# Kernel tuning notes

Measured on AMD Instinct MI355X. Metric: run time of the kernel, lower is better.

The kernel has to match this reference:

```python
import jax, jax.numpy as jnp
import numpy as np

RADIUS = 1.0
NSAMPLE = 1024  # num_votes
EPS = 1e-5     # BatchNorm eps


def _bn2(x, gamma, beta):
    # BatchNorm over [B, C, NS]: stats per channel across (batch, sample)
    m = jnp.mean(x, axis=(0, 2), keepdims=True)
    v = jnp.var(x, axis=(0, 2), keepdims=True)
    return gamma[None, :, None] * (x - m) * jax.lax.rsqrt(v + EPS) + beta[None, :, None]


def _bn1(x, gamma, beta):
    # BatchNorm over [B, C] (conv1d head with length 1): stats across batch
    m = jnp.mean(x, axis=0, keepdims=True)
    v = jnp.var(x, axis=0, keepdims=True)
    return gamma[None, :] * (x - m) * jax.lax.rsqrt(v + EPS) + beta[None, :]


def setup_inputs() -> dict:
    key = jax.random.key(0)
    ks = jax.random.split(key, 16)
    B, N, C = 8, 65536, 256
    def w(k, o, i):
        return jax.random.normal(k, (o, i), jnp.float32) * (1.0 / np.sqrt(i))
    inp = {
        'xyz': jax.random.normal(ks[0], (B, N, 3), jnp.float32),
        'features': jax.random.normal(ks[1], (B, C, N), jnp.float32),
        # shared MLP (conv2d 1x1 + BN + ReLU) x3, input channels = C+3 (use_xyz)
        'w1': w(ks[2], 128, C + 3), 'b1': jnp.zeros(128), 'g1': jnp.ones(128), 'be1': jnp.zeros(128),
        'w2': w(ks[3], 128, 128),   'b2': jnp.zeros(128), 'g2': jnp.ones(128), 'be2': jnp.zeros(128),
        'w3': w(ks[4], 128, 128),   'b3': jnp.zeros(128), 'g3': jnp.ones(128), 'be3': jnp.zeros(128),
        # conv1d head
        'hw1': w(ks[5], 128, 128), 'hb1': jnp.zeros(128), 'hg1': jnp.ones(128), 'hbe1': jnp.zeros(128),
        'hw2': w(ks[6], 128, 128), 'hb2': jnp.zeros(128), 'hg2': jnp.ones(128), 'hbe2': jnp.zeros(128),
        'hw3': w(ks[7], 12, 128),  'hb3': jnp.zeros(12),
    }
    return inp


def reference(xyz, features, w1, b1, g1, be1, w2, b2, g2, be2, w3, b3, g3, be3,
              hw1, hb1, hg1, hbe1, hw2, hb2, hg2, hbe2, hw3, hb3):
    B, N, _ = xyz.shape
    # FPS with npoint=1 deterministically selects point 0
    center = xyz[:, 0, :]                                   # [B,3]
    d2 = jnp.sum((xyz - center[:, None, :]) ** 2, axis=-1)   # [B,N]
    mask = d2 < RADIUS * RADIUS
    ar = jnp.arange(N)
    # ball query: first NSAMPLE in-radius indices (index order), pad with first hit
    order = jnp.argsort(jnp.where(mask, ar, N + ar), axis=1)[:, :NSAMPLE]  # [B,NS]
    valid = jnp.take_along_axis(mask, order, axis=1)
    inds = jnp.where(valid, order, order[:, :1])              # [B,NS]
    g_xyz = (jnp.take_along_axis(xyz, inds[:, :, None], axis=1) - center[:, None, :]) / RADIUS  # [B,NS,3]
    g_feat = jax.vmap(lambda f, i: f[:, i])(features, inds)    # [B,C,NS]
    g = jnp.concatenate([jnp.swapaxes(g_xyz, 1, 2), g_feat], axis=1)  # [B,C+3,NS]

    def mlp(x, w, b, gm, bt):
        y = jnp.einsum('oc,bcn->bon', w, x) + b[None, :, None]
        return jax.nn.relu(_bn2(y, gm, bt))

    h = mlp(g, w1, b1, g1, be1)
    h = mlp(h, w2, b2, g2, be2)
    h = mlp(h, w3, b3, g3, be3)
    f = jnp.max(h, axis=2)                                    # [B,128] maxpool over nsample

    net = jax.nn.relu(_bn1(f @ hw1.T + hb1, hg1, hbe1))
    net = jax.nn.relu(_bn1(net @ hw2.T + hb2, hg2, hbe2))
    net = net @ hw3.T + hb3                                   # [B,12]

    center_out = center + net[:, 0:3]
    size = net[:, 3:6]
    rot_6d = net[:, 6:12]
    return (center_out, size, rot_6d)
```

## Files before the change

### kernel.cpp

```cpp
#include <hip/hip_runtime.h>
#include <hip/hip_bf16.h>
#include <stdint.h>

#define BATCH 8
#define NPTS  65536
#define CFEAT 256
#define K1    259
#define CH    128
#define NS    1024
#define EPSF  1e-5f
#define INVN  (1.0f / (BATCH * NS))

__device__ __forceinline__ unsigned fenc(float f) {
  unsigned u = __float_as_uint(f);
  return (u & 0x80000000u) ? ~u : (u | 0x80000000u);
}
__device__ __forceinline__ float fdec(unsigned k) {
  unsigned u = (k & 0x80000000u) ? (k & 0x7fffffffu) : ~k;
  return __uint_as_float(u);
}

__global__ __launch_bounds__(1024) void k_select(const float* __restrict__ xyz,
                                                 int* __restrict__ inds,
                                                 float* __restrict__ center) {
  int b = blockIdx.x;
  int tid = threadIdx.x;
  int lane = tid & 63, wid = tid >> 6;
  const float* xb = xyz + (size_t)b * NPTS * 3;
  float cx = xb[0], cy = xb[1], cz = xb[2];
  if (tid < 3) center[b * 3 + tid] = xb[tid];

  __shared__ int wcnt[16];
  int total = 0;
  int* ib = inds + b * NS;

  for (int base = 0; base < NPTS; base += 1024) {
    int i = base + tid;
    float dx = xb[(size_t)i * 3 + 0] - cx;
    float dy = xb[(size_t)i * 3 + 1] - cy;
    float dz = xb[(size_t)i * 3 + 2] - cz;
    float d2 = dx * dx + dy * dy + dz * dz;
    bool pred = d2 < 1.0f;
    unsigned long long bal = __ballot(pred);
    if (lane == 0) wcnt[wid] = (int)__popcll(bal);
    __syncthreads();
    int woff = 0, itot = 0;
#pragma unroll
    for (int w = 0; w < 16; ++w) {
      int c = wcnt[w];
      if (w < wid) woff += c;
      itot += c;
    }
    int pos = total + woff + (int)__popcll(bal & ((1ull << lane) - 1ull));
    if (pred && pos < NS) ib[pos] = i;
    total += itot;
    __syncthreads();
    if (total >= NS) break;
  }
  for (int j = total + tid; j < NS; j += 1024) ib[j] = 0;
}

__global__ __launch_bounds__(256) void k_gather(const float* __restrict__ xyz,
                                                const float* __restrict__ feat,
                                                const int* __restrict__ inds,
                                                const float* __restrict__ center,
                                                float* __restrict__ G) {
  int rk = blockIdx.x;
  int b = rk / K1, k = rk - b * K1;
  const int* ib = inds + b * NS;
  float* gr = G + (size_t)rk * NS;
  if (k < 3) {
    float cv = center[b * 3 + k];
    const float* xb = xyz + (size_t)b * NPTS * 3;
    for (int j = threadIdx.x; j < NS; j += 256)
      gr[j] = xb[(size_t)ib[j] * 3 + k] - cv;
  } else {
    const float* fr = feat + ((size_t)b * CFEAT + (k - 3)) * NPTS;
    for (int j = threadIdx.x; j < NS; j += 256)
      gr[j] = fr[ib[j]];
  }
}

__device__ __forceinline__ void store_and_stats(float* __restrict__ yb,
                                                float* __restrict__ sums,
                                                const float* __restrict__ bias,
                                                float acc[4][4],
                                                int n0, int tx, int ty) {
#pragma unroll
  for (int r = 0; r < 4; ++r) {
    int o = ty * 4 + r;
    float bs = bias[o];
    float4 v = make_float4(acc[r][0] + bs, acc[r][1] + bs,
                           acc[r][2] + bs, acc[r][3] + bs);
    *(float4*)&yb[(size_t)o * NS + n0 + tx * 4] = v;
    float s = v.x + v.y + v.z + v.w;
    float q = v.x * v.x + v.y * v.y + v.z * v.z + v.w * v.w;
    s += __shfl_xor(s, 1, 64); q += __shfl_xor(q, 1, 64);
    s += __shfl_xor(s, 2, 64); q += __shfl_xor(q, 2, 64);
    s += __shfl_xor(s, 4, 64); q += __shfl_xor(q, 4, 64);
    if (tx == 0) {
      atomicAdd(&sums[o], s);
      atomicAdd(&sums[CH + o], q);
    }
  }
}

__global__ __launch_bounds__(256) void k_gemm1(const float* __restrict__ G,
                                               const float* __restrict__ W,
                                               const float* __restrict__ bias,
                                               float* __restrict__ y,
                                               float* __restrict__ sums) {
  __shared__ float Ws[32][132];
  __shared__ float Xs[32][36];
  int b = blockIdx.y;
  int n0 = blockIdx.x * 32;
  int tid = threadIdx.x;

  int tx = tid & 7, ty = tid >> 3;
  float acc[4][4];
#pragma unroll
  for (int r = 0; r < 4; ++r)
#pragma unroll
    for (int j = 0; j < 4; ++j) acc[r][j] = 0.f;

  const float* Gb = G + (size_t)b * K1 * NS;

  for (int k0 = 0; k0 < K1; k0 += 32) {
#pragma unroll
    for (int i = 0; i < 16; ++i) {
      int e = tid + 256 * i;
      int o = e >> 5, kk = e & 31;
      int k = k0 + kk;
      Ws[kk][o] = (k < K1) ? W[o * K1 + k] : 0.f;
    }
#pragma unroll
    for (int i = 0; i < 4; ++i) {
      int e = tid + 256 * i;
      int kk = e >> 5, j = e & 31;
      int k = k0 + kk;
      Xs[kk][j] = (k < K1) ? Gb[(size_t)k * NS + n0 + j] : 0.f;
    }
    __syncthreads();
#pragma unroll
    for (int kk = 0; kk < 32; ++kk) {
      float4 xv = *(const float4*)&Xs[kk][tx * 4];
      float4 wv = *(const float4*)&Ws[kk][ty * 4];
      acc[0][0] += wv.x * xv.x; acc[0][1] += wv.x * xv.y; acc[0][2] += wv.x * xv.z; acc[0][3] += wv.x * xv.w;
      acc[1][0] += wv.y * xv.x; acc[1][1] += wv.y * xv.y; acc[1][2] += wv.y * xv.z; acc[1][3] += wv.y * xv.w;
      acc[2][0] += wv.z * xv.x; acc[2][1] += wv.z * xv.y; acc[2][2] += wv.z * xv.z; acc[2][3] += wv.z * xv.w;
      acc[3][0] += wv.w * xv.x; acc[3][1] += wv.w * xv.y; acc[3][2] += wv.w * xv.z; acc[3][3] += wv.w * xv.w;
    }
    __syncthreads();
  }
  store_and_stats(y + (size_t)b * CH * NS, sums, bias, acc, n0, tx, ty);
}

template <bool LAST>
__global__ __launch_bounds__(256) void k_gemm23(const float* __restrict__ x,
                                                const float* __restrict__ sums_prev,
                                                const float* __restrict__ gamma,
                                                const float* __restrict__ beta,
                                                const float* __restrict__ W,
                                                const float* __restrict__ bias,
                                                float* __restrict__ y,
                                                float* __restrict__ sums_out,
                                                unsigned* __restrict__ maxk,
                                                unsigned* __restrict__ mink) {
  __shared__ float Ws[32][132];
  __shared__ float Xs[32][36];
  __shared__ float scl[CH], shf[CH];
  int b = blockIdx.y;
  int n0 = blockIdx.x * 32;
  int tid = threadIdx.x;
  if (tid < CH) {
    float s = sums_prev[tid], q = sums_prev[CH + tid];
    float mean = s * INVN;
    float var = fmaxf(q * INVN - mean * mean, 0.f);
    float sc = gamma[tid] * rsqrtf(var + EPSF);
    scl[tid] = sc;
    shf[tid] = beta[tid] - mean * sc;
  }
  __syncthreads();

  int tx = tid & 7, ty = tid >> 3;
  float acc[4][4];
#pragma unroll
  for (int r = 0; r < 4; ++r)
#pragma unroll
    for (int j = 0; j < 4; ++j) acc[r][j] = 0.f;

  const float* xb = x + (size_t)b * CH * NS;

  for (int k0 = 0; k0 < CH; k0 += 32) {
#pragma unroll
    for (int i = 0; i < 16; ++i) {
      int e = tid + 256 * i;
      int o = e >> 5, kk = e & 31;
      Ws[kk][o] = W[o * CH + k0 + kk];
    }
#pragma unroll
    for (int i = 0; i < 4; ++i) {
      int e = tid + 256 * i;
      int kk = e >> 5, j = e & 31;
      int k = k0 + kk;
      float v = xb[(size_t)k * NS + n0 + j];
      Xs[kk][j] = fmaxf(scl[k] * v + shf[k], 0.f);
    }
    __syncthreads();
#pragma unroll
    for (int kk = 0; kk < 32; ++kk) {
      float4 xv = *(const float4*)&Xs[kk][tx * 4];
      float4 wv = *(const float4*)&Ws[kk][ty * 4];
      acc[0][0] += wv.x * xv.x; acc[0][1] += wv.x * xv.y; acc[0][2] += wv.x * xv.z; acc[0][3] += wv.x * xv.w;
      acc[1][0] += wv.y * xv.x; acc[1][1] += wv.y * xv.y; acc[1][2] += wv.y * xv.z; acc[1][3] += wv.y * xv.w;
      acc[2][0] += wv.z * xv.x; acc[2][1] += wv.z * xv.y; acc[2][2] += wv.z * xv.z; acc[2][3] += wv.z * xv.w;
      acc[3][0] += wv.w * xv.x; acc[3][1] += wv.w * xv.y; acc[3][2] += wv.w * xv.z; acc[3][3] += wv.w * xv.w;
    }
    __syncthreads();
  }

  if (!LAST) {
    store_and_stats(y + (size_t)b * CH * NS, sums_out, bias, acc, n0, tx, ty);
  } else {
#pragma unroll
    for (int r = 0; r < 4; ++r) {
      int o = ty * 4 + r;
      float bs = bias[o];
      float4 v = make_float4(acc[r][0] + bs, acc[r][1] + bs,
                             acc[r][2] + bs, acc[r][3] + bs);
      float s = v.x + v.y + v.z + v.w;
      float q = v.x * v.x + v.y * v.y + v.z * v.z + v.w * v.w;
      float mx = fmaxf(fmaxf(v.x, v.y), fmaxf(v.z, v.w));
      float mn = fminf(fminf(v.x, v.y), fminf(v.z, v.w));
      s += __shfl_xor(s, 1, 64); q += __shfl_xor(q, 1, 64);
      mx = fmaxf(mx, __shfl_xor(mx, 1, 64)); mn = fminf(mn, __shfl_xor(mn, 1, 64));
      s += __shfl_xor(s, 2, 64); q += __shfl_xor(q, 2, 64);
      mx = fmaxf(mx, __shfl_xor(mx, 2, 64)); mn = fminf(mn, __shfl_xor(mn, 2, 64));
      s += __shfl_xor(s, 4, 64); q += __shfl_xor(q, 4, 64);
      mx = fmaxf(mx, __shfl_xor(mx, 4, 64)); mn = fminf(mn, __shfl_xor(mn, 4, 64));
      if (tx == 0) {
        atomicAdd(&sums_out[o], s);
        atomicAdd(&sums_out[CH + o], q);
        atomicMax(&maxk[b * CH + o], fenc(mx));
        atomicMin(&mink[b * CH + o], fenc(mn));
      }
    }
  }
}

__global__ __launch_bounds__(128) void k_head(const float* __restrict__ sums3,
                                              const float* __restrict__ ga3, const float* __restrict__ be3,
                                              const unsigned* __restrict__ maxk, const unsigned* __restrict__ mink,
                                              const float* __restrict__ hw1, const float* __restrict__ hb1,
                                              const float* __restrict__ hg1, const float* __restrict__ hbe1,
                                              const float* __restrict__ hw2, const float* __restrict__ hb2,
                                              const float* __restrict__ hg2, const float* __restrict__ hbe2,
                                              const float* __restrict__ hw3, const float* __restrict__ hb3,
                                              const float* __restrict__ center,
                                              float* __restrict__ out) {
  __shared__ float A[BATCH * 128];
  __shared__ float Bm[BATCH * 128];
  int c = threadIdx.x;
  {
    float s = sums3[c], q = sums3[CH + c];
    float mean = s * INVN;
    float var = fmaxf(q * INVN - mean * mean, 0.f);
    float sc = ga3[c] * rsqrtf(var + EPSF);
    float sh = be3[c] - mean * sc;
#pragma unroll
    for (int b = 0; b < BATCH; ++b) {
      float ymax = fdec(maxk[b * CH + c]);
      float ymin = fdec(mink[b * CH + c]);
      float ye = (sc >= 0.f) ? ymax : ymin;
      A[b * 128 + c] = fmaxf(sc * ye + sh, 0.f);
    }
  }
  __syncthreads();

  {
    float v[BATCH];
    float bs = hb1[c];
#pragma unroll
    for (int b = 0; b < BATCH; ++b) v[b] = bs;
    const float4* w4 = (const float4*)hw1 + c * 32;
    for (int k4 = 0; k4 < 32; ++k4) {
      float4 w = w4[k4];
#pragma unroll
      for (int b = 0; b < BATCH; ++b) {
        const float* Ar = &A[b * 128 + k4 * 4];
        v[b] += Ar[0] * w.x + Ar[1] * w.y + Ar[2] * w.z + Ar[3] * w.w;
      }
    }
    float m = 0.f;
#pragma unroll
    for (int b = 0; b < BATCH; ++b) m += v[b];
    m *= (1.f / BATCH);
    float var = 0.f;
#pragma unroll
    for (int b = 0; b < BATCH; ++b) { float d = v[b] - m; var += d * d; }
    var *= (1.f / BATCH);
    float r = rsqrtf(var + EPSF);
    float ga = hg1[c], be = hbe1[c];
#pragma unroll
    for (int b = 0; b < BATCH; ++b)
      Bm[b * 128 + c] = fmaxf(ga * (v[b] - m) * r + be, 0.f);
  }
  __syncthreads();

  {
    float v[BATCH];
    float bs = hb2[c];
#pragma unroll
    for (int b = 0; b < BATCH; ++b) v[b] = bs;
    const float4* w4 = (const float4*)hw2 + c * 32;
    for (int k4 = 0; k4 < 32; ++k4) {
      float4 w = w4[k4];
#pragma unroll
      for (int b = 0; b < BATCH; ++b) {
        const float* Br = &Bm[b * 128 + k4 * 4];
        v[b] += Br[0] * w.x + Br[1] * w.y + Br[2] * w.z + Br[3] * w.w;
      }
    }
    float m = 0.f;
#pragma unroll
    for (int b = 0; b < BATCH; ++b) m += v[b];
    m *= (1.f / BATCH);
    float var = 0.f;
#pragma unroll
    for (int b = 0; b < BATCH; ++b) { float d = v[b] - m; var += d * d; }
    var *= (1.f / BATCH);
    float r = rsqrtf(var + EPSF);
    float ga = hg2[c], be = hbe2[c];
#pragma unroll
    for (int b = 0; b < BATCH; ++b)
      A[b * 128 + c] = fmaxf(ga * (v[b] - m) * r + be, 0.f);
  }
  __syncthreads();

  if (c < 96) {
    int b = c / 12, j = c % 12;
    float o = hb3[j];
    const float4* w4 = (const float4*)hw3 + j * 32;
    for (int k4 = 0; k4 < 32; ++k4) {
      float4 w = w4[k4];
      const float* Ar = &A[b * 128 + k4 * 4];
      o += Ar[0] * w.x + Ar[1] * w.y + Ar[2] * w.z + Ar[3] * w.w;
    }
    if (j < 3)      out[b * 3 + j] = center[b * 3 + j] + o;
    else if (j < 6) out[24 + b * 3 + (j - 3)] = o;
    else            out[48 + b * 6 + (j - 6)] = o;
  }
}

extern "C" void kernel_launch(void* const* d_in, const int* in_sizes, int n_in,
                              void* d_out, int out_size, void* d_ws, size_t ws_size,
                              hipStream_t stream) {
  const float* xyz  = (const float*)d_in[0];
  const float* feat = (const float*)d_in[1];
  const float* w1   = (const float*)d_in[2];
  const float* b1   = (const float*)d_in[3];
  const float* ga1  = (const float*)d_in[4];
  const float* be1  = (const float*)d_in[5];
  const float* w2   = (const float*)d_in[6];
  const float* b2   = (const float*)d_in[7];
  const float* ga2  = (const float*)d_in[8];
  const float* be2  = (const float*)d_in[9];
  const float* w3   = (const float*)d_in[10];
  const float* b3   = (const float*)d_in[11];
  const float* ga3  = (const float*)d_in[12];
  const float* be3  = (const float*)d_in[13];
  const float* hw1  = (const float*)d_in[14];
  const float* hb1  = (const float*)d_in[15];
  const float* hg1  = (const float*)d_in[16];
  const float* hbe1 = (const float*)d_in[17];
  const float* hw2  = (const float*)d_in[18];
  const float* hb2  = (const float*)d_in[19];
  const float* hg2  = (const float*)d_in[20];
  const float* hbe2 = (const float*)d_in[21];
  const float* hw3  = (const float*)d_in[22];
  const float* hb3  = (const float*)d_in[23];
  float* out = (float*)d_out;

  char* ws = (char*)d_ws;
  size_t off = 0;
  auto alloc = [&](size_t bytes) -> void* {
    void* p = ws + off;
    off = (off + bytes + 255) & ~(size_t)255;
    return p;
  };
  float*    sums1 = (float*)alloc(2 * CH * 4);
  float*    sums2 = (float*)alloc(2 * CH * 4);
  float*    sums3 = (float*)alloc(2 * CH * 4);
  unsigned* maxk  = (unsigned*)alloc((size_t)BATCH * CH * 4);
  unsigned* mink  = (unsigned*)alloc((size_t)BATCH * CH * 4);
  int*      inds  = (int*)alloc((size_t)BATCH * NS * 4);
  float*    center= (float*)alloc(BATCH * 3 * 4);
  float*    G     = (float*)alloc((size_t)BATCH * K1 * NS * 4);
  float*    y1    = (float*)alloc((size_t)BATCH * CH * NS * 4);
  float*    y2    = (float*)alloc((size_t)BATCH * CH * NS * 4);

  hipMemsetAsync(sums1, 0, (size_t)((char*)mink - (char*)sums1), stream);
  hipMemsetAsync(mink, 0xFF, (size_t)BATCH * CH * 4, stream);

  k_select<<<dim3(BATCH), dim3(1024), 0, stream>>>(xyz, inds, center);
  k_gather<<<dim3(BATCH * K1), dim3(256), 0, stream>>>(xyz, feat, inds, center, G);
  k_gemm1<<<dim3(NS / 32, BATCH), dim3(256), 0, stream>>>(G, w1, b1, y1, sums1);
  k_gemm23<false><<<dim3(NS / 32, BATCH), dim3(256), 0, stream>>>(y1, sums1, ga1, be1,
                                                                  w2, b2, y2, sums2,
                                                                  nullptr, nullptr);
  k_gemm23<true><<<dim3(NS / 32, BATCH), dim3(256), 0, stream>>>(y2, sums2, ga2, be2,
                                                                 w3, b3, nullptr, sums3,
                                                                 maxk, mink);
  k_head<<<dim3(1), dim3(128), 0, stream>>>(sums3, ga3, be3, maxk, mink,
                                            hw1, hb1, hg1, hbe1,
                                            hw2, hb2, hg2, hbe2, hw3, hb3,
                                            center, out);
}
```

Baseline: 872.1 us.

## Fuse point gather into first GEMM and fold workspace init into select

Removes the separate gather kernel and the intermediate G buffer. k_gemm1 now gathers the xyz offsets and feature columns for its 32 samples directly into a full-K shared tile, padded to 288 rows. The two memsets are replaced by zero/fill stores done in block 0 of k_select. k_gemm23 also preloads its whole normalized input tile into shared memory once, instead of reloading it per K slice. This saves the G write and read and two launches. In exchange, the random feature gathers run inside only 256 GEMM blocks, which have less latency hiding, and the larger shared-memory footprint may lower occupancy.

New measurement: 851.4 us. 1.02x faster.

```diff
diff --git a/kernel.cpp b/kernel.cpp
--- a/kernel.cpp
+++ b/kernel.cpp
@@ -6,6 +6,7 @@
 #define NPTS  65536
 #define CFEAT 256
 #define K1    259
+#define K1PAD 288
 #define CH    128
 #define NS    1024
 #define EPSF  1e-5f
@@ -22,10 +23,19 @@
 
 __global__ __launch_bounds__(1024) void k_select(const float* __restrict__ xyz,
                                                  int* __restrict__ inds,
-                                                 float* __restrict__ center) {
+                                                 float* __restrict__ center,
+                                                 float* __restrict__ sums,
+                                                 unsigned* __restrict__ maxk,
+                                                 unsigned* __restrict__ mink) {
   int b = blockIdx.x;
   int tid = threadIdx.x;
   int lane = tid & 63, wid = tid >> 6;
+
+  if (b == 0) {
+    if (tid < 3 * 2 * CH) sums[tid] = 0.f;
+    if (tid < BATCH * CH) { maxk[tid] = 0u; mink[tid] = 0xFFFFFFFFu; }
+  }
+
   const float* xb = xyz + (size_t)b * NPTS * 3;
   float cx = xb[0], cy = xb[1], cz = xb[2];
   if (tid < 3) center[b * 3 + tid] = xb[tid];
@@ -58,27 +68,6 @@
     if (total >= NS) break;
   }
   for (int j = total + tid; j < NS; j += 1024) ib[j] = 0;
-}
-
-__global__ __launch_bounds__(256) void k_gather(const float* __restrict__ xyz,
-                                                const float* __restrict__ feat,
-                                                const int* __restrict__ inds,
-                                                const float* __restrict__ center,
-                                                float* __restrict__ G) {
-  int rk = blockIdx.x;
-  int b = rk / K1, k = rk - b * K1;
-  const int* ib = inds + b * NS;
-  float* gr = G + (size_t)rk * NS;
-  if (k < 3) {
-    float cv = center[b * 3 + k];
-    const float* xb = xyz + (size_t)b * NPTS * 3;
-    for (int j = threadIdx.x; j < NS; j += 256)
-      gr[j] = xb[(size_t)ib[j] * 3 + k] - cv;
-  } else {
-    const float* fr = feat + ((size_t)b * CFEAT + (k - 3)) * NPTS;
-    for (int j = threadIdx.x; j < NS; j += 256)
-      gr[j] = fr[ib[j]];
-  }
 }
 
 __device__ __forceinline__ void store_and_stats(float* __restrict__ yb,
@@ -105,16 +94,41 @@
   }
 }
 
-__global__ __launch_bounds__(256) void k_gemm1(const float* __restrict__ G,
+__global__ __launch_bounds__(256) void k_gemm1(const float* __restrict__ xyz,
+                                               const float* __restrict__ feat,
+                                               const int* __restrict__ inds,
+                                               const float* __restrict__ center,
                                                const float* __restrict__ W,
                                                const float* __restrict__ bias,
                                                float* __restrict__ y,
                                                float* __restrict__ sums) {
   __shared__ float Ws[32][132];
-  __shared__ float Xs[32][36];
+  __shared__ float Xs[K1PAD][36];
+  __shared__ int   ids[32];
+  __shared__ float cenl[3];
   int b = blockIdx.y;
   int n0 = blockIdx.x * 32;
   int tid = threadIdx.x;
+  if (tid < 32) ids[tid] = inds[b * NS + n0 + tid];
+  if (tid < 3)  cenl[tid] = center[b * 3 + tid];
+  __syncthreads();
+
+  const float* featb = feat + (size_t)b * CFEAT * NPTS;
+  const float* xyzb  = xyz + (size_t)b * NPTS * 3;
+
+  if (tid < 96) {
+    int k = tid >> 5, j = tid & 31;
+    Xs[k][j] = xyzb[(size_t)ids[j] * 3 + k] - cenl[k];
+  }
+#pragma unroll 8
+  for (int e = tid; e < CFEAT * 32; e += 256) {
+    int k = e >> 5, j = e & 31;
+    Xs[3 + k][j] = featb[(size_t)k * NPTS + ids[j]];
+  }
+#pragma unroll
+  for (int e = tid; e < 29 * 32; e += 256) {
+    Xs[K1 + (e >> 5)][e & 31] = 0.f;
+  }
 
   int tx = tid & 7, ty = tid >> 3;
   float acc[4][4];
@@ -123,9 +137,7 @@
 #pragma unroll
     for (int j = 0; j < 4; ++j) acc[r][j] = 0.f;
 
-  const float* Gb = G + (size_t)b * K1 * NS;
-
-  for (int k0 = 0; k0 < K1; k0 += 32) {
+  for (int k0 = 0; k0 < K1PAD; k0 += 32) {
 #pragma unroll
     for (int i = 0; i < 16; ++i) {
       int e = tid + 256 * i;
@@ -133,17 +145,10 @@
       int k = k0 + kk;
       Ws[kk][o] = (k < K1) ? W[o * K1 + k] : 0.f;
     }
-#pragma unroll
-    for (int i = 0; i < 4; ++i) {
-      int e = tid + 256 * i;
-      int kk = e >> 5, j = e & 31;
-      int k = k0 + kk;
-      Xs[kk][j] = (k < K1) ? Gb[(size_t)k * NS + n0 + j] : 0.f;
-    }
     __syncthreads();
 #pragma unroll
     for (int kk = 0; kk < 32; ++kk) {
-      float4 xv = *(const float4*)&Xs[kk][tx * 4];
+      float4 xv = *(const float4*)&Xs[k0 + kk][tx * 4];
       float4 wv = *(const float4*)&Ws[kk][ty * 4];
       acc[0][0] += wv.x * xv.x; acc[0][1] += wv.x * xv.y; acc[0][2] += wv.x * xv.z; acc[0][3] += wv.x * xv.w;
       acc[1][0] += wv.y * xv.x; acc[1][1] += wv.y * xv.y; acc[1][2] += wv.y * xv.z; acc[1][3] += wv.y * xv.w;
@@ -167,7 +172,7 @@
                                                 unsigned* __restrict__ maxk,
                                                 unsigned* __restrict__ mink) {
   __shared__ float Ws[32][132];
-  __shared__ float Xs[32][36];
+  __shared__ float Xs[CH][36];
   __shared__ float scl[CH], shf[CH];
   int b = blockIdx.y;
   int n0 = blockIdx.x * 32;
@@ -182,14 +187,20 @@
   }
   __syncthreads();
 
+  const float* xb = x + (size_t)b * CH * NS;
+#pragma unroll
+  for (int e = tid; e < CH * 32; e += 256) {
+    int k = e >> 5, j = e & 31;
+    float v = xb[(size_t)k * NS + n0 + j];
+    Xs[k][j] = fmaxf(scl[k] * v + shf[k], 0.f);
+  }
+
   int tx = tid & 7, ty = tid >> 3;
   float acc[4][4];
 #pragma unroll
   for (int r = 0; r < 4; ++r)
 #pragma unroll
     for (int j = 0; j < 4; ++j) acc[r][j] = 0.f;
-
-  const float* xb = x + (size_t)b * CH * NS;
 
   for (int k0 = 0; k0 < CH; k0 += 32) {
 #pragma unroll
@@ -198,18 +209,10 @@
       int o = e >> 5, kk = e & 31;
       Ws[kk][o] = W[o * CH + k0 + kk];
     }
-#pragma unroll
-    for (int i = 0; i < 4; ++i) {
-      int e = tid + 256 * i;
-      int kk = e >> 5, j = e & 31;
-      int k = k0 + kk;
-      float v = xb[(size_t)k * NS + n0 + j];
-      Xs[kk][j] = fmaxf(scl[k] * v + shf[k], 0.f);
-    }
     __syncthreads();
 #pragma unroll
     for (int kk = 0; kk < 32; ++kk) {
-      float4 xv = *(const float4*)&Xs[kk][tx * 4];
+      float4 xv = *(const float4*)&Xs[k0 + kk][tx * 4];
       float4 wv = *(const float4*)&Ws[kk][ty * 4];
       acc[0][0] += wv.x * xv.x; acc[0][1] += wv.x * xv.y; acc[0][2] += wv.x * xv.z; acc[0][3] += wv.x * xv.w;
       acc[1][0] += wv.y * xv.x; acc[1][1] += wv.y * xv.y; acc[1][2] += wv.y * xv.z; acc[1][3] += wv.y * xv.w;
@@ -395,16 +398,13 @@
   unsigned* mink  = (unsigned*)alloc((size_t)BATCH * CH * 4);
   int*      inds  = (int*)alloc((size_t)BATCH * NS * 4);
   float*    center= (float*)alloc(BATCH * 3 * 4);
-  float*    G     = (float*)alloc((size_t)BATCH * K1 * NS * 4);
   float*    y1    = (float*)alloc((size_t)BATCH * CH * NS * 4);
   float*    y2    = (float*)alloc((size_t)BATCH * CH * NS * 4);
 
-  hipMemsetAsync(sums1, 0, (size_t)((char*)mink - (char*)sums1), stream);
-  hipMemsetAsync(mink, 0xFF, (size_t)BATCH * CH * 4, stream);
-
-  k_select<<<dim3(BATCH), dim3(1024), 0, stream>>>(xyz, inds, center);
-  k_gather<<<dim3(BATCH * K1), dim3(256), 0, stream>>>(xyz, feat, inds, center, G);
-  k_gemm1<<<dim3(NS / 32, BATCH), dim3(256), 0, stream>>>(G, w1, b1, y1, sums1);
+  k_select<<<dim3(BATCH), dim3(1024), 0, stream>>>(xyz, inds, center,
+                                                   sums1, maxk, mink);
+  k_gemm1<<<dim3(NS / 32, BATCH), dim3(256), 0, stream>>>(xyz, feat, inds, center,
+                                                          w1, b1, y1, sums1);
   k_gemm23<false><<<dim3(NS / 32, BATCH), dim3(256), 0, stream>>>(y1, sums1, ga1, be1,
                                                                   w2, b2, y2, sums2,
                                                                   nullptr, nullptr);
```
